# Kernel optimization log

Measured on AMD Instinct MI355X. Metric: run time of the kernel, lower is better.

The kernel has to match this reference:

```python
import jax, jax.numpy as jnp
import numpy as np
import math

NUM_HEADS = 16
ROPE_BASE = 10000.0
SLIDING_WINDOW = 512  # note: original triu-then-tril composition makes the mask empty (no-op)


def _rope_cos_sin(seq_len, head_dim, dtype):
    inv_freq = 1.0 / (ROPE_BASE ** (jnp.arange(0, head_dim, 2, dtype=jnp.float32) / head_dim))
    t = jnp.arange(seq_len, dtype=jnp.float32)
    freqs = t[:, None] * inv_freq[None, :]          # [S, D/2]
    emb = jnp.concatenate([freqs, freqs], axis=-1)  # [S, D]
    # reshape to broadcast over [B, S, H, D]
    return jnp.cos(emb)[None, :, None, :].astype(dtype), jnp.sin(emb)[None, :, None, :].astype(dtype)


def _rotate_half(x):
    x1, x2 = jnp.split(x, 2, axis=-1)
    return jnp.concatenate([-x2, x1], axis=-1)


def setup_inputs() -> dict:
    key = jax.random.key(0)
    ks = jax.random.split(key, 9)
    B, S, E = 2, 2048, 2048
    sc = 1.0 / math.sqrt(E)
    return {
        "hidden_states": jax.random.normal(ks[0], (B, S, E), dtype=jnp.float32),
        "Wq": jax.random.normal(ks[1], (E, E), dtype=jnp.float32) * sc,
        "bq": jax.random.normal(ks[2], (E,), dtype=jnp.float32) * 0.01,
        "Wk": jax.random.normal(ks[3], (E, E), dtype=jnp.float32) * sc,
        "bk": jax.random.normal(ks[4], (E,), dtype=jnp.float32) * 0.01,
        "Wv": jax.random.normal(ks[5], (E, E), dtype=jnp.float32) * sc,
        "bv": jax.random.normal(ks[6], (E,), dtype=jnp.float32) * 0.01,
        "Wo": jax.random.normal(ks[7], (E, E), dtype=jnp.float32) * sc,
        "bo": jax.random.normal(ks[8], (E,), dtype=jnp.float32) * 0.01,
    }


def reference(hidden_states, Wq, bq, Wk, bk, Wv, bv, Wo, bo):
    B, S, E = hidden_states.shape
    H = NUM_HEADS
    D = E // H
    q = (hidden_states @ Wq.T + bq).reshape(B, S, H, D)
    k = (hidden_states @ Wk.T + bk).reshape(B, S, H, D)
    v = (hidden_states @ Wv.T + bv).reshape(B, S, H, D)

    cos, sin = _rope_cos_sin(S, D, q.dtype)
    q = q * cos + _rotate_half(q) * sin
    k = k * cos + _rotate_half(k) * sin

    scale = 1.0 / math.sqrt(D)
    scores = jnp.einsum("bqhd,bkhd->bhqk", q, k) * scale  # [B,H,S,S]
    # Faithful to source: triu(ones, +w) followed by tril(..., -w) is empty -> mask is a no-op.
    attn = jax.nn.softmax(scores, axis=-1)
    out = jnp.einsum("bhqk,bkhd->bqhd", attn, v).reshape(B, S, E)
    return out @ Wo.T + bo
```

## Files before the change

kernel.cpp:

```cpp
#include <hip/hip_runtime.h>
#include <hip/hip_bf16.h>

#define B_ 2
#define S_ 2048
#define E_ 2048
#define H_ 16
#define D_ 128
#define M_ (B_*S_)
#define NQKV_ (3*E_)

typedef __attribute__((ext_vector_type(8))) short bf16x8;
typedef __attribute__((ext_vector_type(4))) float f32x4;
typedef __attribute__((ext_vector_type(4))) unsigned short u16x4;
typedef __attribute__((ext_vector_type(2))) unsigned u32x2;

__device__ __forceinline__ unsigned short f2bf(float f) {
  union { float f; unsigned u; } v; v.f = f;
  unsigned r = v.u + 0x7fffu + ((v.u >> 16) & 1u);
  return (unsigned short)(r >> 16);
}
__device__ __forceinline__ float bf2f(unsigned short h) {
  union { unsigned u; float f; } v; v.u = ((unsigned)h) << 16;
  return v.f;
}

__device__ __forceinline__ void gload_lds16(const void* g, void* l) {
  __builtin_amdgcn_global_load_lds(
      (const __attribute__((address_space(1))) unsigned*)g,
      (__attribute__((address_space(3))) unsigned*)l, 16, 0, 0);
}

__global__ __launch_bounds__(256) void prep_kernel(
    const float* __restrict__ hs,
    const float* __restrict__ Wq, const float* __restrict__ Wk, const float* __restrict__ Wv,
    const float* __restrict__ Wo,
    const float* __restrict__ bq, const float* __restrict__ bk, const float* __restrict__ bv,
    unsigned short* __restrict__ hsb, unsigned short* __restrict__ Wqkv,
    unsigned short* __restrict__ Wob, float* __restrict__ biasqkv,
    float* __restrict__ cosT, float* __restrict__ sinT)
{
  const int seg = blockIdx.y;
  const int t0 = blockIdx.x * 256 + threadIdx.x;
  const int stride = gridDim.x * 256;
  if (seg == 0) {
    const int n = (M_*E_)/4;
    for (int i = t0; i < n; i += stride) {
      f32x4 v = ((const f32x4*)hs)[i];
      u16x4 o; o[0]=f2bf(v[0]); o[1]=f2bf(v[1]); o[2]=f2bf(v[2]); o[3]=f2bf(v[3]);
      ((u16x4*)hsb)[i] = o;
    }
  } else if (seg == 1) {
    const int n = (3*E_*E_)/4;
    for (int i = t0; i < n; i += stride) {
      int e4 = i << 2;
      int r = e4 >> 11;
      int k = e4 & 2047;
      const float* src = (r < E_) ? (Wq + ((size_t)r << 11) + k)
                       : (r < 2*E_) ? (Wk + ((size_t)(r - E_) << 11) + k)
                       : (Wv + ((size_t)(r - 2*E_) << 11) + k);
      f32x4 v = *(const f32x4*)src;
      u16x4 o; o[0]=f2bf(v[0]); o[1]=f2bf(v[1]); o[2]=f2bf(v[2]); o[3]=f2bf(v[3]);
      ((u16x4*)Wqkv)[i] = o;
    }
  } else if (seg == 2) {
    const int n = (E_*E_)/4;
    for (int i = t0; i < n; i += stride) {
      f32x4 v = ((const f32x4*)Wo)[i];
      u16x4 o; o[0]=f2bf(v[0]); o[1]=f2bf(v[1]); o[2]=f2bf(v[2]); o[3]=f2bf(v[3]);
      ((u16x4*)Wob)[i] = o;
    }
  } else if (seg == 3) {
    for (int i = t0; i < NQKV_; i += stride)
      biasqkv[i] = (i < E_) ? bq[i] : (i < 2*E_) ? bk[i - E_] : bv[i - 2*E_];
  } else {
    for (int i = t0; i < S_*64; i += stride) {
      int j = i & 63, s = i >> 6;
      float inv = exp2f(-(float)j * (13.287712379549449f / 64.0f));
      float ang = (float)s * inv;
      cosT[i] = cosf(ang);
      sinT[i] = sinf(ang);
    }
  }
}

#define STAGE8(basePtr, BUF, AB, KS, KT) do { \
    unsigned short* dst_ = lds + (BUF)*32768 + (AB)*16384 + (KS)*8192; \
    const unsigned short* src_ = (basePtr) + (KT)*64 + (KS)*32; \
    _Pragma("unroll") \
    for (int j_ = 0; j_ < 2; ++j_) { \
      int cc_ = (j_ << 9) + tid; \
      int row_ = cc_ >> 2, c2_ = cc_ & 3; \
      int sc_ = c2_ ^ ((row_ >> 1) & 3); \
      gload_lds16(src_ + (size_t)row_*K + sc_*8, (char*)dst_ + cc_*16); \
    } } while(0)

#define LOADA8(MH, KS, BUF) do { \
    const unsigned short* Ab_ = lds + (BUF)*32768 + (KS)*8192; \
    _Pragma("unroll") \
    for (int j_ = 0; j_ < 4; ++j_) { \
      int row_ = wr*128 + ((MH)*4 + j_)*16 + l15; \
      af[j_] = *(const bf16x8*)(Ab_ + row_*32 + ((l4 ^ ((row_>>1)&3)) << 3)); \
    } } while(0)

#define LOADB8(KS, BUF) do { \
    const unsigned short* Bb_ = lds + (BUF)*32768 + 16384 + (KS)*8192; \
    _Pragma("unroll") \
    for (int j_ = 0; j_ < 4; ++j_) { \
      int row_ = wc*64 + j_*16 + l15; \
      bf[j_] = *(const bf16x8*)(Bb_ + row_*32 + ((l4 ^ ((row_>>1)&3)) << 3)); \
    } } while(0)

#define MFMAQ(MH) do { \
    _Pragma("unroll") \
    for (int mm_ = 0; mm_ < 4; ++mm_) \
      _Pragma("unroll") \
      for (int nn_ = 0; nn_ < 4; ++nn_) \
        acc[(MH)*4+mm_][nn_] = __builtin_amdgcn_mfma_f32_16x16x32_bf16(af[mm_], bf[nn_], acc[(MH)*4+mm_][nn_], 0,0,0); \
  } while(0)

#define WVM6 asm volatile("s_waitcnt vmcnt(6)" ::: "memory")
#define WVM0 asm volatile("s_waitcnt vmcnt(0)" ::: "memory")

#define PHASE(MH, KS, BUF, ISSUE, WAITV) do { \
    LOADA8(MH, KS, BUF); \
    if ((MH) == 0) LOADB8(KS, BUF); \
    ISSUE; \
    __builtin_amdgcn_sched_barrier(0); \
    __builtin_amdgcn_s_barrier(); \
    asm volatile("s_waitcnt lgkmcnt(0)" ::: "memory"); \
    __builtin_amdgcn_sched_barrier(0); \
    __builtin_amdgcn_s_setprio(1); \
    MFMAQ(MH); \
    __builtin_amdgcn_s_setprio(0); \
    WAITV; \
    __builtin_amdgcn_s_barrier(); \
  } while(0)

__global__ __launch_bounds__(512, 2) void gemm8(
    const unsigned short* __restrict__ A,
    const unsigned short* __restrict__ Bm,
    const float* __restrict__ bias,
    unsigned short* __restrict__ Cv,
    int M, int N, int K, int ldc)
{
  __shared__ __align__(16) unsigned short lds[65536];
  const int tid = threadIdx.x;
  const int lane = tid & 63;
  const int w = tid >> 6;
  const int wr = w >> 2, wc = w & 3;
  const int l15 = lane & 15, l4 = lane >> 4;

  const int ntile = N >> 8;
  int wg = blockIdx.x;
  const int cpx = gridDim.x >> 3;
  wg = (wg & 7) * cpx + (wg >> 3);
  const int tm = wg / ntile, tn = wg % ntile;

  const unsigned short* Abase = A + ((size_t)tm*256)*K;
  const unsigned short* Bbase = Bm + ((size_t)tn*256)*K;

  f32x4 acc[8][4] = {};
  bf16x8 af[4], bf[4];

  const int NITER = K >> 7;

  STAGE8(Bbase, 0, 1, 0, 0); STAGE8(Abase, 0, 0, 0, 0);
  STAGE8(Bbase, 0, 1, 1, 0); STAGE8(Abase, 0, 0, 1, 0);
  STAGE8(Bbase, 1, 1, 0, 1); STAGE8(Abase, 1, 0, 0, 1);
  STAGE8(Bbase, 1, 1, 1, 1);
  __builtin_amdgcn_sched_barrier(0);
  WVM6;
  __builtin_amdgcn_s_barrier();

  for (int i = 0; i < NITER; ++i) {
    const int t1k = 2*i + 1, t2k = 2*i + 2, t3k = 2*i + 3;
    const bool nl = (i < NITER - 1);
    PHASE(0, 0, 0, STAGE8(Abase, 1, 0, 1, t1k), );
    PHASE(1, 0, 0, if (nl) STAGE8(Bbase, 0, 1, 0, t2k), );
    PHASE(0, 1, 0, if (nl) STAGE8(Abase, 0, 0, 0, t2k), );
    PHASE(1, 1, 0, if (nl) STAGE8(Bbase, 0, 1, 1, t2k), if (nl) WVM6; else WVM0);
    PHASE(0, 0, 1, if (nl) STAGE8(Abase, 0, 0, 1, t2k), );
    PHASE(1, 0, 1, if (nl) STAGE8(Bbase, 1, 1, 0, t3k), );
    PHASE(0, 1, 1, if (nl) STAGE8(Abase, 1, 0, 0, t3k), );
    PHASE(1, 1, 1, if (nl) STAGE8(Bbase, 1, 1, 1, t3k), if (nl) WVM6);
  }

  #pragma unroll
  for (int mt = 0; mt < 8; ++mt) {
    #pragma unroll
    for (int nt = 0; nt < 4; ++nt) {
      int colg = tn*256 + wc*64 + nt*16 + l15;
      float bvv = bias[colg];
      #pragma unroll
      for (int r = 0; r < 4; ++r) {
        int rowg = tm*256 + wr*128 + mt*16 + l4*4 + r;
        Cv[(size_t)rowg*ldc + colg] = f2bf(acc[mt][nt][r] + bvv);
      }
    }
  }
}

#define STGA(BUFP, TKT, KS) do { \
    unsigned short* dst_ = lds + (BUFP)*24576 + (KS)*4096; \
    const unsigned short* src_ = Abase + (TKT)*64 + (KS)*32; \
    int cc_ = tid; int row_ = cc_ >> 2, c2_ = cc_ & 3; \
    int sc_ = c2_ ^ ((row_ >> 1) & 3); \
    gload_lds16(src_ + (size_t)row_*K + sc_*8, (char*)dst_ + cc_*16); \
  } while(0)

#define STGB(BUFP, TKT, KS) do { \
    unsigned short* dst_ = lds + (BUFP)*24576 + 8192 + (KS)*8192; \
    const unsigned short* src_ = Bbase + (TKT)*64 + (KS)*32; \
    _Pragma("unroll") \
    for (int j_ = 0; j_ < 2; ++j_) { \
      int cc_ = (j_ << 9) + tid; int row_ = cc_ >> 2, c2_ = cc_ & 3; \
      int sc_ = c2_ ^ ((row_ >> 1) & 3); \
      gload_lds16(src_ + (size_t)row_*K + sc_*8, (char*)dst_ + cc_*16); \
    } } while(0)

#define PHA(KS, BUF, ISSUE, WAITV) do { \
    { const unsigned short* Ab_ = lds + (BUF)*24576 + (KS)*4096; \
      _Pragma("unroll") \
      for (int j_ = 0; j_ < 4; ++j_) { \
        int row_ = wr*64 + j_*16 + l15; \
        af[j_] = *(const bf16x8*)(Ab_ + row_*32 + ((l4 ^ ((row_>>1)&3)) << 3)); } \
      const unsigned short* Bb_ = lds + (BUF)*24576 + 8192 + (KS)*8192; \
      _Pragma("unroll") \
      for (int j_ = 0; j_ < 4; ++j_) { \
        int row_ = wc*64 + j_*16 + l15; \
        bf[j_] = *(const bf16x8*)(Bb_ + row_*32 + ((l4 ^ ((row_>>1)&3)) << 3)); } } \
    ISSUE; \
    __builtin_amdgcn_sched_barrier(0); \
    __builtin_amdgcn_s_barrier(); \
    asm volatile("s_waitcnt lgkmcnt(0)" ::: "memory"); \
    __builtin_amdgcn_sched_barrier(0); \
    __builtin_amdgcn_s_setprio(1); \
    _Pragma("unroll") \
    for (int mm_ = 0; mm_ < 4; ++mm_) \
      _Pragma("unroll") \
      for (int nn_ = 0; nn_ < 4; ++nn_) \
        acc[mm_][nn_] = __builtin_amdgcn_mfma_f32_16x16x32_bf16(af[mm_], bf[nn_], acc[mm_][nn_], 0,0,0); \
    __builtin_amdgcn_s_setprio(0); \
    WAITV; \
    __builtin_amdgcn_s_barrier(); \
  } while(0)

template<int OUT_F32>
__global__ __launch_bounds__(512, 2) void gemmA(
    const unsigned short* __restrict__ A,
    const unsigned short* __restrict__ Bm,
    const float* __restrict__ bias,
    void* __restrict__ Cv,
    int M, int N, int K, int ldc)
{
  __shared__ __align__(16) unsigned short lds[73728];
  const int tid = threadIdx.x;
  const int lane = tid & 63;
  const int w = tid >> 6;
  const int wr = w >> 2, wc = w & 3;
  const int l15 = lane & 15, l4 = lane >> 4;

  const int ntile = N >> 8;
  int wg = blockIdx.x;
  const int cpx = gridDim.x >> 3;
  wg = (wg & 7) * cpx + (wg >> 3);
  const int tm = wg / ntile, tn = wg % ntile;

  const unsigned short* Abase = A + ((size_t)tm*128)*K;
  const unsigned short* Bbase = Bm + ((size_t)tn*256)*K;

  f32x4 acc[4][4] = {};
  bf16x8 af[4], bf[4];

  const int NT = K >> 6;

  STGA(0,0,0); STGB(0,0,0); STGA(0,0,1); STGB(0,0,1);
  STGA(1,1,0); STGB(1,1,0); STGA(1,1,1); STGB(1,1,1);
  __builtin_amdgcn_sched_barrier(0);
  asm volatile("s_waitcnt vmcnt(6)" ::: "memory");
  __builtin_amdgcn_s_barrier();
  __builtin_amdgcn_sched_barrier(0);

  int bufc = 0, bufn = 2;
  for (int i = 0; i < NT; ++i) {
    const bool st = (i + 2 < NT);
    const bool more = (i + 1 < NT);
    PHA(0, bufc, if (st) { STGA(bufn, i+2, 0); STGB(bufn, i+2, 0); }, );
    PHA(1, bufc, if (st) { STGA(bufn, i+2, 1); STGB(bufn, i+2, 1); },
        if (st) { asm volatile("s_waitcnt vmcnt(6)" ::: "memory"); }
        else if (more) { asm volatile("s_waitcnt vmcnt(0)" ::: "memory"); });
    bufc = (bufc + 1 == 3) ? 0 : bufc + 1;
    bufn = (bufn + 1 == 3) ? 0 : bufn + 1;
  }

  #pragma unroll
  for (int mt = 0; mt < 4; ++mt) {
    #pragma unroll
    for (int nt = 0; nt < 4; ++nt) {
      int colg = tn*256 + wc*64 + nt*16 + l15;
      float bvv = bias[colg];
      #pragma unroll
      for (int r = 0; r < 4; ++r) {
        int rowg = tm*128 + wr*64 + mt*16 + l4*4 + r;
        float v = acc[mt][nt][r] + bvv;
        if (OUT_F32) ((float*)Cv)[(size_t)rowg*ldc + colg] = v;
        else ((unsigned short*)Cv)[(size_t)rowg*ldc + colg] = f2bf(v);
      }
    }
  }
}

__global__ __launch_bounds__(256) void rope_kernel(
    unsigned short* __restrict__ qkv, const float* __restrict__ cosT, const float* __restrict__ sinT)
{
  int t = blockIdx.x*256 + threadIdx.x;
  int i  = t & 63;
  int h  = (t >> 6) & 15;
  int m  = t >> 10;
  int s  = m & (S_-1);
  float c = cosT[s*64 + i], sn = sinT[s*64 + i];
  const float scale = 0.08838834764831845f * 1.4426950408889634f;
  size_t base = (size_t)m*NQKV_ + h*128;
  float q1 = bf2f(qkv[base+i]), q2 = bf2f(qkv[base+64+i]);
  qkv[base+i]    = f2bf((q1*c - q2*sn)*scale);
  qkv[base+64+i] = f2bf((q2*c + q1*sn)*scale);
  size_t kb = base + E_;
  float k1 = bf2f(qkv[kb+i]), k2 = bf2f(qkv[kb+64+i]);
  qkv[kb+i]    = f2bf(k1*c - k2*sn);
  qkv[kb+64+i] = f2bf(k2*c + k1*sn);
}

__global__ __launch_bounds__(256) void transv_kernel(
    const unsigned short* __restrict__ qkv, unsigned short* __restrict__ Vt)
{
  __shared__ unsigned short t[32][33];
  int bid = blockIdx.x;
  int st = bid & 63;
  int dt = (bid >> 6) & 3;
  int bh = bid >> 8;
  int b = bh >> 4, h = bh & 15;
  int tx = threadIdx.x & 31, ty = threadIdx.x >> 5;
  #pragma unroll
  for (int j = 0; j < 4; ++j) {
    int r = ty + j*8;
    t[r][tx] = qkv[(size_t)(b*S_ + st*32 + r)*NQKV_ + 2*E_ + h*128 + dt*32 + tx];
  }
  __syncthreads();
  #pragma unroll
  for (int j = 0; j < 4; ++j) {
    int r = ty + j*8;
    Vt[((size_t)bh*D_ + dt*32 + r)*S_ + st*32 + tx] = t[tx][r];
  }
}

__global__ __launch_bounds__(256, 2) void attn_kernel(
    const unsigned short* __restrict__ qkv, const unsigned short* __restrict__ Vt,
    unsigned short* __restrict__ Ao)
{
  __shared__ unsigned short lK[2][64*128];
  __shared__ unsigned short lV[2][128*64];
  __shared__ __align__(16) unsigned short lP[4*32*64];
  int bid = blockIdx.x;
  bid = (bid & 7)*64 + (bid >> 3);
  const int qt = bid & 15;
  const int bh = bid >> 4;
  const int b = bh >> 4, h = bh & 15;
  const int tid = threadIdx.x, lane = tid & 63, w = tid >> 6;
  const int l15 = lane & 15, l4 = lane >> 4;

  bf16x8 qf[2][4];
  #pragma unroll
  for (int g = 0; g < 2; ++g) {
    const int qrow = qt*128 + w*32 + g*16 + l15;
    const unsigned short* qp = qkv + (size_t)(b*S_ + qrow)*NQKV_ + h*128 + l4*8;
    #pragma unroll
    for (int f = 0; f < 4; ++f) qf[g][f] = *(const bf16x8*)(qp + f*32);
  }

  f32x4 O[2][8];
  #pragma unroll
  for (int g = 0; g < 2; ++g)
    #pragma unroll
    for (int i = 0; i < 8; ++i) O[g][i] = (f32x4){0.f,0.f,0.f,0.f};
  float mx[2] = {-1e30f,-1e30f}, lsum[2] = {0.f,0.f};

  unsigned short* myP = lP + w*(32*64);
  const int ksw = (l15 & 7) << 3;
  const size_t kbase = (size_t)b*S_*NQKV_ + E_ + (size_t)h*128;
  const size_t vbase = (size_t)bh*D_*S_;

  #define ASTAGE(bi, ktile) do { \
    _Pragma("unroll") \
    for (int i_ = 0; i_ < 4; ++i_) { \
      int cc_ = i_*256 + tid; \
      int row_ = cc_ >> 4, col_ = cc_ & 15; \
      int scol_ = col_ ^ (row_ & 7); \
      gload_lds16(qkv + kbase + (size_t)((ktile)*64 + row_)*NQKV_ + scol_*8, \
                  (char*)(&lK[bi][0]) + cc_*16); \
    } \
    _Pragma("unroll") \
    for (int i_ = 0; i_ < 4; ++i_) { \
      int cc_ = i_*256 + tid; \
      int row_ = cc_ >> 3, col_ = cc_ & 7; \
      int scol_ = col_ ^ ((row_ & 7) ^ ((row_ >> 3) & 7)); \
      gload_lds16(Vt + vbase + (size_t)row_*S_ + (ktile)*64 + scol_*8, \
                  (char*)(&lV[bi][0]) + cc_*16); \
    } } while(0)

  ASTAGE(0, 0);
  asm volatile("s_waitcnt vmcnt(0)" ::: "memory");
  __syncthreads();

  for (int it = 0; it < S_/64; ++it) {
    const int cur = it & 1;
    if (it + 1 < S_/64) ASTAGE(cur ^ 1, it + 1);
    __builtin_amdgcn_sched_barrier(0);

    f32x4 sfr[2][4];
    __builtin_amdgcn_s_setprio(1);
    #pragma unroll
    for (int nf = 0; nf < 4; ++nf) {
      f32x4 s0 = (f32x4){0.f,0.f,0.f,0.f};
      f32x4 s1 = (f32x4){0.f,0.f,0.f,0.f};
      #pragma unroll
      for (int ks = 0; ks < 4; ++ks) {
        int row = nf*16 + l15;
        int ch = (ks*4 + l4) ^ (row & 7);
        bf16x8 kf = *(const bf16x8*)(&lK[cur][0] + row*128 + ch*8);
        s0 = __builtin_amdgcn_mfma_f32_16x16x32_bf16(kf, qf[0][ks], s0, 0, 0, 0);
        s1 = __builtin_amdgcn_mfma_f32_16x16x32_bf16(kf, qf[1][ks], s1, 0, 0, 0);
      }
      sfr[0][nf] = s0; sfr[1][nf] = s1;
    }
    __builtin_amdgcn_s_setprio(0);

    float vm[2];
    #pragma unroll
    for (int g = 0; g < 2; ++g) {
      float v = -1e30f;
      #pragma unroll
      for (int nf = 0; nf < 4; ++nf)
        #pragma unroll
        for (int r = 0; r < 4; ++r) v = fmaxf(v, sfr[g][nf][r]);
      v = fmaxf(v, __shfl_xor(v, 16, 64));
      v = fmaxf(v, __shfl_xor(v, 32, 64));
      vm[g] = v;
    }

    if (__any((vm[0] > mx[0] + 8.0f) || (vm[1] > mx[1] + 8.0f))) {
      #pragma unroll
      for (int g = 0; g < 2; ++g) {
        float mn = fmaxf(mx[g], vm[g]);
        float al = __builtin_amdgcn_exp2f(mx[g] - mn);
        mx[g] = mn;
        lsum[g] *= al;
        #pragma unroll
        for (int r = 0; r < 4; ++r) {
          float ar = __shfl(al, (lane & 48) + l4*4 + r, 64);
          #pragma unroll
          for (int df = 0; df < 8; ++df) O[g][df][r] *= ar;
        }
      }
    }

    #pragma unroll
    for (int g = 0; g < 2; ++g) {
      float ps = 0.f;
      #pragma unroll
      for (int nf = 0; nf < 4; ++nf) {
        #pragma unroll
        for (int r = 0; r < 4; ++r) {
          float p = __builtin_amdgcn_exp2f(sfr[g][nf][r] - mx[g]);
          sfr[g][nf][r] = p;
          ps += p;
        }
      }
      ps += __shfl_xor(ps, 16, 64);
      ps += __shfl_xor(ps, 32, 64);
      lsum[g] += ps;
    }

    #pragma unroll
    for (int g = 0; g < 2; ++g) {
      #pragma unroll
      for (int nf = 0; nf < 4; ++nf) {
        unsigned lo, hi;
        asm("v_cvt_pk_bf16_f32 %0, %1, %2" : "=v"(lo) : "v"(sfr[g][nf][0]), "v"(sfr[g][nf][1]));
        asm("v_cvt_pk_bf16_f32 %0, %1, %2" : "=v"(hi) : "v"(sfr[g][nf][2]), "v"(sfr[g][nf][3]));
        int k0 = (nf*16 + l4*4) ^ ksw;
        u32x2 val; val[0] = lo; val[1] = hi;
        *(u32x2*)(myP + (g*16 + l15)*64 + k0) = val;
      }
    }
    asm volatile("s_waitcnt lgkmcnt(0)" ::: "memory");

    __builtin_amdgcn_s_setprio(1);
    #pragma unroll
    for (int ks2 = 0; ks2 < 2; ++ks2) {
      int kk = (ks2*32 + l4*8) ^ ksw;
      bf16x8 pf0 = *(const bf16x8*)(myP + l15*64 + kk);
      bf16x8 pf1 = *(const bf16x8*)(myP + (16 + l15)*64 + kk);
      #pragma unroll
      for (int df = 0; df < 8; ++df) {
        int row = df*16 + l15;
        int ch = (ks2*4 + l4) ^ ((row & 7) ^ ((row >> 3) & 7));
        bf16x8 vf = *(const bf16x8*)(&lV[cur][0] + row*64 + ch*8);
        O[0][df] = __builtin_amdgcn_mfma_f32_16x16x32_bf16(pf0, vf, O[0][df], 0, 0, 0);
        O[1][df] = __builtin_amdgcn_mfma_f32_16x16x32_bf16(pf1, vf, O[1][df], 0, 0, 0);
      }
    }
    __builtin_amdgcn_s_setprio(0);
    asm volatile("s_waitcnt vmcnt(0)" ::: "memory");
    __syncthreads();
  }

  #pragma unroll
  for (int g = 0; g < 2; ++g) {
    float linv = 1.0f / lsum[g];
    float inv[4];
    #pragma unroll
    for (int r = 0; r < 4; ++r) inv[r] = __shfl(linv, (lane & 48) + l4*4 + r, 64);
    #pragma unroll
    for (int df = 0; df < 8; ++df) {
      int colg = h*128 + df*16 + l15;
      #pragma unroll
      for (int r = 0; r < 4; ++r) {
        int rowg = qt*128 + w*32 + g*16 + l4*4 + r;
        Ao[(size_t)(b*S_ + rowg)*E_ + colg] = f2bf(O[g][df][r] * inv[r]);
      }
    }
  }
}

extern "C" void kernel_launch(void* const* d_in, const int* in_sizes, int n_in,
                              void* d_out, int out_size, void* d_ws, size_t ws_size,
                              hipStream_t stream) {
  const float* hs = (const float*)d_in[0];
  const float* Wq = (const float*)d_in[1];
  const float* bq = (const float*)d_in[2];
  const float* Wk = (const float*)d_in[3];
  const float* bk = (const float*)d_in[4];
  const float* Wv = (const float*)d_in[5];
  const float* bv = (const float*)d_in[6];
  const float* Wo = (const float*)d_in[7];
  const float* bo = (const float*)d_in[8];
  float* out = (float*)d_out;

  char* p = (char*)d_ws;
  auto alloc = [&](size_t bytes) { char* r = p; p += (bytes + 255) & ~(size_t)255; return r; };
  unsigned short* hsb  = (unsigned short*)alloc((size_t)M_*E_*2);
  unsigned short* Wqkv = (unsigned short*)alloc((size_t)NQKV_*E_*2);
  unsigned short* Wob  = (unsigned short*)alloc((size_t)E_*E_*2);
  unsigned short* qkv  = (unsigned short*)alloc((size_t)M_*NQKV_*2);
  unsigned short* Vt   = (unsigned short*)alloc((size_t)B_*H_*D_*S_*2);
  unsigned short* Ao   = (unsigned short*)alloc((size_t)M_*E_*2);
  float* biasqkv = (float*)alloc((size_t)NQKV_*4);
  float* cosT = (float*)alloc((size_t)S_*64*4);
  float* sinT = (float*)alloc((size_t)S_*64*4);

  prep_kernel<<<dim3(2048, 5), 256, 0, stream>>>(hs, Wq, Wk, Wv, Wo, bq, bk, bv,
      hsb, Wqkv, Wob, biasqkv, cosT, sinT);
  gemm8<<<dim3((M_/256)*(2*E_/256)), 512, 0, stream>>>(
      hsb, Wqkv, biasqkv, qkv, M_, 2*E_, E_, NQKV_);
  gemmA<0><<<dim3((M_/128)*(E_/256)), 512, 0, stream>>>(
      hsb, Wqkv + (size_t)2*E_*E_, biasqkv + 2*E_, qkv + 2*E_, M_, E_, E_, NQKV_);
  rope_kernel<<<dim3((M_*H_*64)/256), 256, 0, stream>>>(qkv, cosT, sinT);
  transv_kernel<<<dim3(B_*H_*(D_/32)*(S_/32)), 256, 0, stream>>>(qkv, Vt);
  attn_kernel<<<dim3(B_*H_*(S_/128)), 256, 0, stream>>>(qkv, Vt, Ao);
  gemmA<1><<<dim3((M_/128)*(E_/256)), 512, 0, stream>>>(
      Ao, Wob, bo, out, M_, E_, E_, E_);
}
```

Baseline: 274.4 us.

## Replace phase-interleaved GEMM pipelines with simpler per-tile double/triple buffering loops

Both GEMM kernels drop the hand-scheduled 8-phase (gemm8) and 2-phase (gemmA) loops, which used per-phase barriers, priority bumps and sched_barriers. In their place is a straightforward loop: issue the global-to-LDS loads for the next tile, run all MFMAs on the current buffer, then wait and barrier once per tile. gemm8 moves from a finer-grained quad-buffer layout to plain double buffering and waits for vmcnt(0) every tile. This cuts barrier count and scheduling constraints, but it weakens the overlap between memory and compute and leaves the compiler free to interleave LDS reads and MFMAs as it likes.

```diff
diff --git a/kernel.cpp b/kernel.cpp
--- a/kernel.cpp
+++ b/kernel.cpp
@@ -94,47 +94,21 @@
       gload_lds16(src_ + (size_t)row_*K + sc_*8, (char*)dst_ + cc_*16); \
     } } while(0)
 
-#define LOADA8(MH, KS, BUF) do { \
+#define LDA8(DST, MH, KS, BUF) do { \
     const unsigned short* Ab_ = lds + (BUF)*32768 + (KS)*8192; \
     _Pragma("unroll") \
     for (int j_ = 0; j_ < 4; ++j_) { \
       int row_ = wr*128 + ((MH)*4 + j_)*16 + l15; \
-      af[j_] = *(const bf16x8*)(Ab_ + row_*32 + ((l4 ^ ((row_>>1)&3)) << 3)); \
+      DST[j_] = *(const bf16x8*)(Ab_ + row_*32 + ((l4 ^ ((row_>>1)&3)) << 3)); \
     } } while(0)
 
-#define LOADB8(KS, BUF) do { \
+#define LDB8(DST, KS, BUF) do { \
     const unsigned short* Bb_ = lds + (BUF)*32768 + 16384 + (KS)*8192; \
     _Pragma("unroll") \
     for (int j_ = 0; j_ < 4; ++j_) { \
       int row_ = wc*64 + j_*16 + l15; \
-      bf[j_] = *(const bf16x8*)(Bb_ + row_*32 + ((l4 ^ ((row_>>1)&3)) << 3)); \
+      DST[j_] = *(const bf16x8*)(Bb_ + row_*32 + ((l4 ^ ((row_>>1)&3)) << 3)); \
     } } while(0)
-
-#define MFMAQ(MH) do { \
-    _Pragma("unroll") \
-    for (int mm_ = 0; mm_ < 4; ++mm_) \
-      _Pragma("unroll") \
-      for (int nn_ = 0; nn_ < 4; ++nn_) \
-        acc[(MH)*4+mm_][nn_] = __builtin_amdgcn_mfma_f32_16x16x32_bf16(af[mm_], bf[nn_], acc[(MH)*4+mm_][nn_], 0,0,0); \
-  } while(0)
-
-#define WVM6 asm volatile("s_waitcnt vmcnt(6)" ::: "memory")
-#define WVM0 asm volatile("s_waitcnt vmcnt(0)" ::: "memory")
-
-#define PHASE(MH, KS, BUF, ISSUE, WAITV) do { \
-    LOADA8(MH, KS, BUF); \
-    if ((MH) == 0) LOADB8(KS, BUF); \
-    ISSUE; \
-    __builtin_amdgcn_sched_barrier(0); \
-    __builtin_amdgcn_s_barrier(); \
-    asm volatile("s_waitcnt lgkmcnt(0)" ::: "memory"); \
-    __builtin_amdgcn_sched_barrier(0); \
-    __builtin_amdgcn_s_setprio(1); \
-    MFMAQ(MH); \
-    __builtin_amdgcn_s_setprio(0); \
-    WAITV; \
-    __builtin_amdgcn_s_barrier(); \
-  } while(0)
 
 __global__ __launch_bounds__(512, 2) void gemm8(
     const unsigned short* __restrict__ A,
@@ -160,29 +134,44 @@
   const unsigned short* Bbase = Bm + ((size_t)tn*256)*K;
 
   f32x4 acc[8][4] = {};
-  bf16x8 af[4], bf[4];
-
-  const int NITER = K >> 7;
+
+  const int NT = K >> 6;
 
   STAGE8(Bbase, 0, 1, 0, 0); STAGE8(Abase, 0, 0, 0, 0);
   STAGE8(Bbase, 0, 1, 1, 0); STAGE8(Abase, 0, 0, 1, 0);
-  STAGE8(Bbase, 1, 1, 0, 1); STAGE8(Abase, 1, 0, 0, 1);
-  STAGE8(Bbase, 1, 1, 1, 1);
   __builtin_amdgcn_sched_barrier(0);
-  WVM6;
+  asm volatile("s_waitcnt vmcnt(0)" ::: "memory");
   __builtin_amdgcn_s_barrier();
 
-  for (int i = 0; i < NITER; ++i) {
-    const int t1k = 2*i + 1, t2k = 2*i + 2, t3k = 2*i + 3;
-    const bool nl = (i < NITER - 1);
-    PHASE(0, 0, 0, STAGE8(Abase, 1, 0, 1, t1k), );
-    PHASE(1, 0, 0, if (nl) STAGE8(Bbase, 0, 1, 0, t2k), );
-    PHASE(0, 1, 0, if (nl) STAGE8(Abase, 0, 0, 0, t2k), );
-    PHASE(1, 1, 0, if (nl) STAGE8(Bbase, 0, 1, 1, t2k), if (nl) WVM6; else WVM0);
-    PHASE(0, 0, 1, if (nl) STAGE8(Abase, 0, 0, 1, t2k), );
-    PHASE(1, 0, 1, if (nl) STAGE8(Bbase, 1, 1, 0, t3k), );
-    PHASE(0, 1, 1, if (nl) STAGE8(Abase, 1, 0, 0, t3k), );
-    PHASE(1, 1, 1, if (nl) STAGE8(Bbase, 1, 1, 1, t3k), if (nl) WVM6);
+  for (int t = 0; t < NT; ++t) {
+    const int cb = t & 1;
+    const bool more = (t + 1 < NT);
+    if (more) {
+      STAGE8(Bbase, cb^1, 1, 0, t+1); STAGE8(Abase, cb^1, 0, 0, t+1);
+      STAGE8(Bbase, cb^1, 1, 1, t+1); STAGE8(Abase, cb^1, 0, 1, t+1);
+    }
+    __builtin_amdgcn_sched_barrier(0);
+    #pragma unroll
+    for (int ks = 0; ks < 2; ++ks) {
+      bf16x8 a0[4], a1[4], bv[4];
+      LDA8(a0, 0, ks, cb);
+      LDA8(a1, 1, ks, cb);
+      LDB8(bv, ks, cb);
+      #pragma unroll
+      for (int mm = 0; mm < 4; ++mm)
+        #pragma unroll
+        for (int nn = 0; nn < 4; ++nn)
+          acc[mm][nn] = __builtin_amdgcn_mfma_f32_16x16x32_bf16(a0[mm], bv[nn], acc[mm][nn], 0,0,0);
+      #pragma unroll
+      for (int mm = 0; mm < 4; ++mm)
+        #pragma unroll
+        for (int nn = 0; nn < 4; ++nn)
+          acc[4+mm][nn] = __builtin_amdgcn_mfma_f32_16x16x32_bf16(a1[mm], bv[nn], acc[4+mm][nn], 0,0,0);
+    }
+    if (more) {
+      asm volatile("s_waitcnt vmcnt(0)" ::: "memory");
+      __builtin_amdgcn_s_barrier();
+    }
   }
 
   #pragma unroll
@@ -217,33 +206,6 @@
       int sc_ = c2_ ^ ((row_ >> 1) & 3); \
       gload_lds16(src_ + (size_t)row_*K + sc_*8, (char*)dst_ + cc_*16); \
     } } while(0)
-
-#define PHA(KS, BUF, ISSUE, WAITV) do { \
-    { const unsigned short* Ab_ = lds + (BUF)*24576 + (KS)*4096; \
-      _Pragma("unroll") \
-      for (int j_ = 0; j_ < 4; ++j_) { \
-        int row_ = wr*64 + j_*16 + l15; \
-        af[j_] = *(const bf16x8*)(Ab_ + row_*32 + ((l4 ^ ((row_>>1)&3)) << 3)); } \
-      const unsigned short* Bb_ = lds + (BUF)*24576 + 8192 + (KS)*8192; \
-      _Pragma("unroll") \
-      for (int j_ = 0; j_ < 4; ++j_) { \
-        int row_ = wc*64 + j_*16 + l15; \
-        bf[j_] = *(const bf16x8*)(Bb_ + row_*32 + ((l4 ^ ((row_>>1)&3)) << 3)); } } \
-    ISSUE; \
-    __builtin_amdgcn_sched_barrier(0); \
-    __builtin_amdgcn_s_barrier(); \
-    asm volatile("s_waitcnt lgkmcnt(0)" ::: "memory"); \
-    __builtin_amdgcn_sched_barrier(0); \
-    __builtin_amdgcn_s_setprio(1); \
-    _Pragma("unroll") \
-    for (int mm_ = 0; mm_ < 4; ++mm_) \
-      _Pragma("unroll") \
-      for (int nn_ = 0; nn_ < 4; ++nn_) \
-        acc[mm_][nn_] = __builtin_amdgcn_mfma_f32_16x16x32_bf16(af[mm_], bf[nn_], acc[mm_][nn_], 0,0,0); \
-    __builtin_amdgcn_s_setprio(0); \
-    WAITV; \
-    __builtin_amdgcn_s_barrier(); \
-  } while(0)
 
 template<int OUT_F32>
 __global__ __launch_bounds__(512, 2) void gemmA(
@@ -270,7 +232,6 @@
   const unsigned short* Bbase = Bm + ((size_t)tn*256)*K;
 
   f32x4 acc[4][4] = {};
-  bf16x8 af[4], bf[4];
 
   const int NT = K >> 6;
 
@@ -279,16 +240,35 @@
   __builtin_amdgcn_sched_barrier(0);
   asm volatile("s_waitcnt vmcnt(6)" ::: "memory");
   __builtin_amdgcn_s_barrier();
-  __builtin_amdgcn_sched_barrier(0);
 
   int bufc = 0, bufn = 2;
   for (int i = 0; i < NT; ++i) {
     const bool st = (i + 2 < NT);
     const bool more = (i + 1 < NT);
-    PHA(0, bufc, if (st) { STGA(bufn, i+2, 0); STGB(bufn, i+2, 0); }, );
-    PHA(1, bufc, if (st) { STGA(bufn, i+2, 1); STGB(bufn, i+2, 1); },
-        if (st) { asm volatile("s_waitcnt vmcnt(6)" ::: "memory"); }
-        else if (more) { asm volatile("s_waitcnt vmcnt(0)" ::: "memory"); });
+    if (st) { STGA(bufn, i+2, 0); STGB(bufn, i+2, 0); STGA(bufn, i+2, 1); STGB(bufn, i+2, 1); }
+    __builtin_amdgcn_sched_barrier(0);
+    #pragma unroll
+    for (int ks = 0; ks < 2; ++ks) {
+      bf16x8 af[4], bv[4];
+      { const unsigned short* Ab_ = lds + bufc*24576 + ks*4096;
+        #pragma unroll
+        for (int j = 0; j < 4; ++j) {
+          int row = wr*64 + j*16 + l15;
+          af[j] = *(const bf16x8*)(Ab_ + row*32 + ((l4 ^ ((row>>1)&3)) << 3)); }
+        const unsigned short* Bb_ = lds + bufc*24576 + 8192 + ks*8192;
+        #pragma unroll
+        for (int j = 0; j < 4; ++j) {
+          int row = wc*64 + j*16 + l15;
+          bv[j] = *(const bf16x8*)(Bb_ + row*32 + ((l4 ^ ((row>>1)&3)) << 3)); } }
+      #pragma unroll
+      for (int mm = 0; mm < 4; ++mm)
+        #pragma unroll
+        for (int nn = 0; nn < 4; ++nn)
+          acc[mm][nn] = __builtin_amdgcn_mfma_f32_16x16x32_bf16(af[mm], bv[nn], acc[mm][nn], 0,0,0);
+    }
+    if (st)       { asm volatile("s_waitcnt vmcnt(6)" ::: "memory"); }
+    else if (more){ asm volatile("s_waitcnt vmcnt(0)" ::: "memory"); }
+    if (more) __builtin_amdgcn_s_barrier();
     bufc = (bufc + 1 == 3) ? 0 : bufc + 1;
     bufn = (bufn + 1 == 3) ? 0 : bufn + 1;
   }
```

After: 276.4 us. No clear change (+0.7%).
